# Performance work log

Measured on AMD Instinct MI355X. Metric: run time of the kernel, lower is better.

Reference implementation:

```python
import jax, jax.numpy as jnp
import numpy as np

S_LIST = (0.015, 0.02, 0.04, 0.08)
EPS = 1e-6
LOG_EPS = float(np.log(EPS))


def _ema_filtfilt(x, s):
    """scipy.signal.filtfilt([s], [1, s-1], x, axis=-1, padtype=None).

    Forward pass: y[n] = (1-s)*y[n-1] + s*x[n], with scipy's lfilter_zi*x[0]
    initial condition, which makes y[0] = x[0] exactly. Then the same filter
    is run backward (flip, filter, flip), again with y2[0] = (flipped y)[0].
    Implemented as a parallel linear-recurrence via associative_scan.
    """
    def one_pass(v):
        a = jnp.full_like(v, 1.0 - s).at[..., 0].set(0.0)
        b = (s * v).at[..., 0].set(v[..., 0])
        def comb(c1, c2):
            a1, b1 = c1
            a2, b2 = c2
            return a1 * a2, b1 * a2 + b2
        _, y = jax.lax.associative_scan(comb, (a, b), axis=-1)
        return y

    y = one_pass(x)                       # forward
    y = jnp.flip(one_pass(jnp.flip(y, axis=-1)), axis=-1)  # backward
    return y


def setup_inputs() -> dict:
    key = jax.random.key(0)
    ks = jax.random.split(key, 5)
    B, C, F, T = 16, 1, 256, 4096
    K = len(S_LIST)
    x = jax.random.uniform(ks[0], (B, C, F, T), dtype=jnp.float32)
    log_alpha = jnp.log(jax.random.normal(ks[1], (F,), dtype=jnp.float32) * 0.1 + 1.0)
    log_delta = jnp.log(jax.random.normal(ks[2], (F,), dtype=jnp.float32) * 0.1 + 1.0)
    log_r = jnp.log(jax.random.normal(ks[3], (F,), dtype=jnp.float32) * 0.1 + 1.0)
    z_ks = jax.random.normal(ks[4], (K, F), dtype=jnp.float32) * 0.1 + np.log(1.0 / K)
    return {"x": x, "log_alpha": log_alpha, "log_delta": log_delta,
            "log_r": log_r, "z_ks": z_ks}


def reference(x, log_alpha, log_delta, log_r, z_ks):
    # per-frequency params broadcast over [B, C, F, T]
    alpha = jnp.exp(log_alpha)[None, None, :, None]
    delta = jnp.exp(log_delta)[None, None, :, None]
    r = jnp.exp(log_r)[None, None, :, None]
    ez = jnp.exp(z_ks)
    w_ks = ez / jnp.sum(ez)  # [K, F], normalized over ALL entries (as in source)

    # multi-scale filtfilt smoothers; scipy path is detached from autodiff
    smoothers = jnp.stack([_ema_filtfilt(x, s) for s in S_LIST])  # [K,B,C,F,T]
    smoothers = jax.lax.stop_gradient(smoothers)

    M = jnp.einsum('kf,kbcft->bcft', w_ks, smoothers)
    M = jnp.exp(-alpha * (LOG_EPS + jnp.log1p(M / EPS)))
    return (x * M + delta) ** r - delta ** r
```

## Files before the change

kernel.cpp:

```cpp
#include <hip/hip_runtime.h>
#include <math.h>

#define T_DIM 4096
#define F_DIM 256
#define NROWS 4096
#define CHUNK 16
#define LOG2E 1.4426950408889634f

typedef float v2f __attribute__((ext_vector_type(2)));

__device__ __forceinline__ float fexp2(float v) { return __builtin_amdgcn_exp2f(v); }
__device__ __forceinline__ float flog2(float v) { return __builtin_amdgcn_logf(v); }
__device__ __forceinline__ float fexp(float v)  { return fexp2(v * LOG2E); }

__host__ __device__ constexpr float cpow(float b, int e) {
    float r = 1.0f;
    for (int i = 0; i < e; ++i) r *= b;
    return r;
}

template<int N> struct PT { float v[N]; };
template<int N>
__host__ __device__ constexpr PT<N> mk_pows(float a) {
    PT<N> t{}; float p = 1.0f;
    for (int i = 0; i < N; ++i) { t.v[i] = p; p *= a; }
    return t;
}

__device__ __forceinline__ v2f shfl_up2(v2f v, int d) {
    v2f r; r.x = __shfl_up(v.x, d, 64); r.y = __shfl_up(v.y, d, 64); return r;
}
__device__ __forceinline__ v2f shfl_down2(v2f v, int d) {
    v2f r; r.x = __shfl_down(v.x, d, 64); r.y = __shfl_down(v.y, d, 64); return r;
}

template<int K0, int K1>
__device__ __forceinline__ void smooth_pair(const float xv[CHUNK], v2f y[CHUNK],
                                            int tid, int lane, int wid, v2f* sE)
{
    constexpr float SL0 = (K0==0)?0.015f:(K0==1)?0.02f:(K0==2)?0.04f:0.08f;
    constexpr float SL1 = (K1==0)?0.015f:(K1==1)?0.02f:(K1==2)?0.04f:0.08f;
    constexpr float a0 = 1.0f - SL0, a1 = 1.0f - SL1;
    constexpr float A0 = cpow(a0, CHUNK), A1 = cpow(a1, CHUNK);
    constexpr float A64_0 = cpow(a0, 64*CHUNK), A64_1 = cpow(a1, 64*CHUNK);
    constexpr PT<CHUNK+1> P0 = mk_pows<CHUNK+1>(a0);
    constexpr PT<CHUNK+1> P1 = mk_pows<CHUNK+1>(a1);
    constexpr PT<33> PA0 = mk_pows<33>(A0);
    constexpr PT<33> PA1 = mk_pows<33>(A1);

    const v2f av = {a0, a1};
    const v2f sv = {SL0, SL1};
    const v2f A64v = {A64_0, A64_1};
    const float lgA0 = flog2(A0), lgA1 = flog2(A1);
    const v2f zero = {0.0f, 0.0f};

    {
        v2f x0 = {xv[0], xv[0]};
        y[0] = (tid == 0) ? x0 : (sv * x0);
    }
    #pragma unroll
    for (int i = 1; i < CHUNK; ++i) {
        v2f xi = {xv[i], xv[i]};
        y[i] = av * y[i-1] + sv * xi;
    }
    {
        v2f e = y[CHUNK-1];
        #pragma unroll
        for (int st = 0; st < 6; ++st) {
            const int d = 1 << st;
            const v2f Ad = {PA0.v[d], PA1.v[d]};
            v2f t = shfl_up2(e, d);
            if (lane >= d) e = Ad * t + e;
        }
        __syncthreads();
        if (lane == 63) sE[wid] = e;
        __syncthreads();
        v2f C = zero;
        for (int j = 0; j < wid; ++j) C = A64v * C + sE[j];
        v2f eex = shfl_up2(e, 1);
        v2f cprev = (lane == 0) ? zero : eex;
        const float fl = (float)lane;
        v2f pAl = {fexp2(fl * lgA0), fexp2(fl * lgA1)};
        v2f c = cprev + pAl * C;
        #pragma unroll
        for (int i = 0; i < CHUNK; ++i) {
            const v2f ap = {P0.v[i+1], P1.v[i+1]};
            y[i] = ap * c + y[i];
        }
    }

    y[CHUNK-1] = (tid == 255) ? y[CHUNK-1] : (sv * y[CHUNK-1]);
    #pragma unroll
    for (int i = CHUNK-2; i >= 0; --i) y[i] = av * y[i+1] + sv * y[i];
    {
        v2f e = y[0];
        #pragma unroll
        for (int st = 0; st < 6; ++st) {
            const int d = 1 << st;
            const v2f Ad = {PA0.v[d], PA1.v[d]};
            v2f t = shfl_down2(e, d);
            if (lane < 64 - d) e = Ad * t + e;
        }
        __syncthreads();
        if (lane == 0) sE[wid] = e;
        __syncthreads();
        v2f C = zero;
        for (int j = 3; j > wid; --j) C = A64v * C + sE[j];
        v2f eex = shfl_down2(e, 1);
        v2f cnext = (lane == 63) ? zero : eex;
        const float frl = (float)(63 - lane);
        v2f pAr = {fexp2(frl * lgA0), fexp2(frl * lgA1)};
        v2f c = cnext + pAr * C;
        #pragma unroll
        for (int i = CHUNK-1; i >= 0; --i) {
            const v2f ap = {P0.v[CHUNK-i], P1.v[CHUNK-i]};
            y[i] = ap * c + y[i];
        }
    }
}

__global__ __launch_bounds__(256, 4)
void pcen_kernel(const float* __restrict__ x,
                 const float* __restrict__ log_alpha,
                 const float* __restrict__ log_delta,
                 const float* __restrict__ log_r,
                 const float* __restrict__ z_ks,
                 float* __restrict__ out)
{
    const int tid  = threadIdx.x;
    const int lane = tid & 63;
    const int wid  = tid >> 6;
    const int rid  = blockIdx.x;
    const int f    = rid & (F_DIM - 1);

    __shared__ float sred[4];
    __shared__ v2f   sE[4];
    __shared__ float sSum;

    float zs = fexp(z_ks[tid])       + fexp(z_ks[tid + 256])
             + fexp(z_ks[tid + 512]) + fexp(z_ks[tid + 768]);
    #pragma unroll
    for (int d = 32; d >= 1; d >>= 1) zs += __shfl_down(zs, d, 64);
    if (lane == 0) sred[wid] = zs;
    __syncthreads();
    if (tid == 0) sSum = sred[0] + sred[1] + sred[2] + sred[3];
    __syncthreads();
    const float invsum = 1.0f / sSum;

    float wk[4];
    #pragma unroll
    for (int k = 0; k < 4; ++k) wk[k] = fexp(z_ks[k * F_DIM + f]) * invsum;
    const float alpha = fexp(log_alpha[f]);
    const float delta = fexp(log_delta[f]);
    const float rr    = fexp(log_r[f]);
    const float dr    = fexp2(rr * flog2(delta));
    const float nalpha = -alpha;

    const size_t base = (size_t)rid * T_DIM + (size_t)tid * CHUNK;
    float xv[CHUNK];
    {
        const float4* xp = (const float4*)(x + base);
        #pragma unroll
        for (int j = 0; j < 4; ++j) {
            float4 v = xp[j];
            xv[4*j+0] = v.x; xv[4*j+1] = v.y; xv[4*j+2] = v.z; xv[4*j+3] = v.w;
        }
    }

    v2f y[CHUNK];
    v2f Mpk[CHUNK];

    smooth_pair<0,1>(xv, y, tid, lane, wid, sE);
    {
        const v2f wv = {wk[0], wk[1]};
        #pragma unroll
        for (int i = 0; i < CHUNK; ++i) Mpk[i] = wv * y[i];
    }
    smooth_pair<2,3>(xv, y, tid, lane, wid, sE);
    {
        const v2f wv = {wk[2], wk[3]};
        #pragma unroll
        for (int i = 0; i < CHUNK; ++i) Mpk[i] = wv * y[i] + Mpk[i];
    }

    float4* op = (float4*)(out + base);
    #pragma unroll
    for (int j = 0; j < 4; ++j) {
        float o[4];
        #pragma unroll
        for (int q = 0; q < 4; ++q) {
            const int i = 4*j + q;
            const float M  = Mpk[i].x + Mpk[i].y;
            const float Mp = fexp2(nalpha * flog2(M + 1.0e-6f));
            const float v  = fmaf(xv[i], Mp, delta);
            o[q] = fexp2(rr * flog2(v)) - dr;
        }
        op[j] = make_float4(o[0], o[1], o[2], o[3]);
    }
}

extern "C" void kernel_launch(void* const* d_in, const int* in_sizes, int n_in,
                              void* d_out, int out_size, void* d_ws, size_t ws_size,
                              hipStream_t stream) {
    const float* x  = (const float*)d_in[0];
    const float* la = (const float*)d_in[1];
    const float* ld = (const float*)d_in[2];
    const float* lr = (const float*)d_in[3];
    const float* zk = (const float*)d_in[4];
    float* o = (float*)d_out;
    (void)in_sizes; (void)n_in; (void)out_size; (void)d_ws; (void)ws_size;
    hipLaunchKernelGGL(pcen_kernel, dim3(NROWS), dim3(256), 0, stream,
                       x, la, ld, lr, zk, o);
}
```

Measured before the change: 39.27 us.

## Interleave all four EMA smoother scans in one pass and hoist input loads

Runs the two smoother pairs side by side instead of one after the other, so the forward and backward scans, shuffles and cross-wave combines happen once for all four scales. This halves the block barriers and doubles independent work per instruction to hide shuffle latency. It also issues the global x loads before the z_ks softmax reduction to overlap memory latency, and drops the first barrier before the forward-pass shared write. The cost is more live registers (two y arrays) at 4 waves per SIMD occupancy.

```diff
diff --git a/kernel.cpp b/kernel.cpp
--- a/kernel.cpp
+++ b/kernel.cpp
@@ -34,90 +34,10 @@
     v2f r; r.x = __shfl_down(v.x, d, 64); r.y = __shfl_down(v.y, d, 64); return r;
 }
 
-template<int K0, int K1>
-__device__ __forceinline__ void smooth_pair(const float xv[CHUNK], v2f y[CHUNK],
-                                            int tid, int lane, int wid, v2f* sE)
-{
-    constexpr float SL0 = (K0==0)?0.015f:(K0==1)?0.02f:(K0==2)?0.04f:0.08f;
-    constexpr float SL1 = (K1==0)?0.015f:(K1==1)?0.02f:(K1==2)?0.04f:0.08f;
-    constexpr float a0 = 1.0f - SL0, a1 = 1.0f - SL1;
-    constexpr float A0 = cpow(a0, CHUNK), A1 = cpow(a1, CHUNK);
-    constexpr float A64_0 = cpow(a0, 64*CHUNK), A64_1 = cpow(a1, 64*CHUNK);
-    constexpr PT<CHUNK+1> P0 = mk_pows<CHUNK+1>(a0);
-    constexpr PT<CHUNK+1> P1 = mk_pows<CHUNK+1>(a1);
-    constexpr PT<33> PA0 = mk_pows<33>(A0);
-    constexpr PT<33> PA1 = mk_pows<33>(A1);
-
-    const v2f av = {a0, a1};
-    const v2f sv = {SL0, SL1};
-    const v2f A64v = {A64_0, A64_1};
-    const float lgA0 = flog2(A0), lgA1 = flog2(A1);
-    const v2f zero = {0.0f, 0.0f};
-
-    {
-        v2f x0 = {xv[0], xv[0]};
-        y[0] = (tid == 0) ? x0 : (sv * x0);
-    }
-    #pragma unroll
-    for (int i = 1; i < CHUNK; ++i) {
-        v2f xi = {xv[i], xv[i]};
-        y[i] = av * y[i-1] + sv * xi;
-    }
-    {
-        v2f e = y[CHUNK-1];
-        #pragma unroll
-        for (int st = 0; st < 6; ++st) {
-            const int d = 1 << st;
-            const v2f Ad = {PA0.v[d], PA1.v[d]};
-            v2f t = shfl_up2(e, d);
-            if (lane >= d) e = Ad * t + e;
-        }
-        __syncthreads();
-        if (lane == 63) sE[wid] = e;
-        __syncthreads();
-        v2f C = zero;
-        for (int j = 0; j < wid; ++j) C = A64v * C + sE[j];
-        v2f eex = shfl_up2(e, 1);
-        v2f cprev = (lane == 0) ? zero : eex;
-        const float fl = (float)lane;
-        v2f pAl = {fexp2(fl * lgA0), fexp2(fl * lgA1)};
-        v2f c = cprev + pAl * C;
-        #pragma unroll
-        for (int i = 0; i < CHUNK; ++i) {
-            const v2f ap = {P0.v[i+1], P1.v[i+1]};
-            y[i] = ap * c + y[i];
-        }
-    }
-
-    y[CHUNK-1] = (tid == 255) ? y[CHUNK-1] : (sv * y[CHUNK-1]);
-    #pragma unroll
-    for (int i = CHUNK-2; i >= 0; --i) y[i] = av * y[i+1] + sv * y[i];
-    {
-        v2f e = y[0];
-        #pragma unroll
-        for (int st = 0; st < 6; ++st) {
-            const int d = 1 << st;
-            const v2f Ad = {PA0.v[d], PA1.v[d]};
-            v2f t = shfl_down2(e, d);
-            if (lane < 64 - d) e = Ad * t + e;
-        }
-        __syncthreads();
-        if (lane == 0) sE[wid] = e;
-        __syncthreads();
-        v2f C = zero;
-        for (int j = 3; j > wid; --j) C = A64v * C + sE[j];
-        v2f eex = shfl_down2(e, 1);
-        v2f cnext = (lane == 63) ? zero : eex;
-        const float frl = (float)(63 - lane);
-        v2f pAr = {fexp2(frl * lgA0), fexp2(frl * lgA1)};
-        v2f c = cnext + pAr * C;
-        #pragma unroll
-        for (int i = CHUNK-1; i >= 0; --i) {
-            const v2f ap = {P0.v[CHUNK-i], P1.v[CHUNK-i]};
-            y[i] = ap * c + y[i];
-        }
-    }
-}
+#define S0 0.015f
+#define S1 0.02f
+#define S2 0.04f
+#define S3 0.08f
 
 __global__ __launch_bounds__(256, 4)
 void pcen_kernel(const float* __restrict__ x,
@@ -134,8 +54,13 @@
     const int f    = rid & (F_DIM - 1);
 
     __shared__ float sred[4];
-    __shared__ v2f   sE[4];
+    __shared__ v2f   sE0[4];
+    __shared__ v2f   sE1[4];
     __shared__ float sSum;
+
+    const size_t base = (size_t)rid * T_DIM + (size_t)tid * CHUNK;
+    const float4* xp = (const float4*)(x + base);
+    float4 xq0 = xp[0], xq1 = xp[1], xq2 = xp[2], xq3 = xp[3];
 
     float zs = fexp(z_ks[tid])       + fexp(z_ks[tid + 256])
              + fexp(z_ks[tid + 512]) + fexp(z_ks[tid + 768]);
@@ -156,41 +81,133 @@
     const float dr    = fexp2(rr * flog2(delta));
     const float nalpha = -alpha;
 
-    const size_t base = (size_t)rid * T_DIM + (size_t)tid * CHUNK;
     float xv[CHUNK];
+    xv[0]=xq0.x; xv[1]=xq0.y; xv[2]=xq0.z; xv[3]=xq0.w;
+    xv[4]=xq1.x; xv[5]=xq1.y; xv[6]=xq1.z; xv[7]=xq1.w;
+    xv[8]=xq2.x; xv[9]=xq2.y; xv[10]=xq2.z; xv[11]=xq2.w;
+    xv[12]=xq3.x; xv[13]=xq3.y; xv[14]=xq3.z; xv[15]=xq3.w;
+
+    constexpr float a0 = 1.0f - S0, a1 = 1.0f - S1, a2 = 1.0f - S2, a3 = 1.0f - S3;
+    constexpr float A0 = cpow(a0, CHUNK), A1 = cpow(a1, CHUNK);
+    constexpr float A2 = cpow(a2, CHUNK), A3 = cpow(a3, CHUNK);
+    constexpr float A64_0 = cpow(a0, 64*CHUNK), A64_1 = cpow(a1, 64*CHUNK);
+    constexpr float A64_2 = cpow(a2, 64*CHUNK), A64_3 = cpow(a3, 64*CHUNK);
+    constexpr PT<CHUNK+1> P0 = mk_pows<CHUNK+1>(a0);
+    constexpr PT<CHUNK+1> P1 = mk_pows<CHUNK+1>(a1);
+    constexpr PT<CHUNK+1> P2 = mk_pows<CHUNK+1>(a2);
+    constexpr PT<CHUNK+1> P3 = mk_pows<CHUNK+1>(a3);
+    constexpr PT<33> PA0 = mk_pows<33>(A0);
+    constexpr PT<33> PA1 = mk_pows<33>(A1);
+    constexpr PT<33> PA2 = mk_pows<33>(A2);
+    constexpr PT<33> PA3 = mk_pows<33>(A3);
+
+    const v2f av01 = {a0, a1}, av23 = {a2, a3};
+    const v2f sv01 = {S0, S1}, sv23 = {S2, S3};
+    const v2f A64v01 = {A64_0, A64_1}, A64v23 = {A64_2, A64_3};
+    const float lgA0 = flog2(A0), lgA1 = flog2(A1), lgA2 = flog2(A2), lgA3 = flog2(A3);
+    const v2f zero = {0.0f, 0.0f};
+
+    v2f y0[CHUNK], y1[CHUNK];
+
     {
-        const float4* xp = (const float4*)(x + base);
-        #pragma unroll
-        for (int j = 0; j < 4; ++j) {
-            float4 v = xp[j];
-            xv[4*j+0] = v.x; xv[4*j+1] = v.y; xv[4*j+2] = v.z; xv[4*j+3] = v.w;
-        }
-    }
-
-    v2f y[CHUNK];
-    v2f Mpk[CHUNK];
-
-    smooth_pair<0,1>(xv, y, tid, lane, wid, sE);
+        v2f x0v = {xv[0], xv[0]};
+        y0[0] = (tid == 0) ? x0v : (sv01 * x0v);
+        y1[0] = (tid == 0) ? x0v : (sv23 * x0v);
+    }
+    #pragma unroll
+    for (int i = 1; i < CHUNK; ++i) {
+        v2f xi = {xv[i], xv[i]};
+        y0[i] = av01 * y0[i-1] + sv01 * xi;
+        y1[i] = av23 * y1[i-1] + sv23 * xi;
+    }
     {
-        const v2f wv = {wk[0], wk[1]};
-        #pragma unroll
-        for (int i = 0; i < CHUNK; ++i) Mpk[i] = wv * y[i];
-    }
-    smooth_pair<2,3>(xv, y, tid, lane, wid, sE);
+        v2f e0 = y0[CHUNK-1], e1 = y1[CHUNK-1];
+        #pragma unroll
+        for (int st = 0; st < 6; ++st) {
+            const int d = 1 << st;
+            const v2f Ad01 = {PA0.v[d], PA1.v[d]};
+            const v2f Ad23 = {PA2.v[d], PA3.v[d]};
+            v2f t0 = shfl_up2(e0, d);
+            v2f t1 = shfl_up2(e1, d);
+            if (lane >= d) { e0 = Ad01 * t0 + e0; e1 = Ad23 * t1 + e1; }
+        }
+        if (lane == 63) { sE0[wid] = e0; sE1[wid] = e1; }
+        __syncthreads();
+        v2f C0 = zero, C1 = zero;
+        for (int j = 0; j < wid; ++j) {
+            C0 = A64v01 * C0 + sE0[j];
+            C1 = A64v23 * C1 + sE1[j];
+        }
+        v2f ex0 = shfl_up2(e0, 1), ex1 = shfl_up2(e1, 1);
+        v2f cp0 = (lane == 0) ? zero : ex0;
+        v2f cp1 = (lane == 0) ? zero : ex1;
+        const float fl = (float)lane;
+        v2f pAl01 = {fexp2(fl * lgA0), fexp2(fl * lgA1)};
+        v2f pAl23 = {fexp2(fl * lgA2), fexp2(fl * lgA3)};
+        v2f c0 = cp0 + pAl01 * C0;
+        v2f c1 = cp1 + pAl23 * C1;
+        #pragma unroll
+        for (int i = 0; i < CHUNK; ++i) {
+            const v2f ap01 = {P0.v[i+1], P1.v[i+1]};
+            const v2f ap23 = {P2.v[i+1], P3.v[i+1]};
+            y0[i] = ap01 * c0 + y0[i];
+            y1[i] = ap23 * c1 + y1[i];
+        }
+    }
+
+    y0[CHUNK-1] = (tid == 255) ? y0[CHUNK-1] : (sv01 * y0[CHUNK-1]);
+    y1[CHUNK-1] = (tid == 255) ? y1[CHUNK-1] : (sv23 * y1[CHUNK-1]);
+    #pragma unroll
+    for (int i = CHUNK-2; i >= 0; --i) {
+        y0[i] = av01 * y0[i+1] + sv01 * y0[i];
+        y1[i] = av23 * y1[i+1] + sv23 * y1[i];
+    }
     {
-        const v2f wv = {wk[2], wk[3]};
-        #pragma unroll
-        for (int i = 0; i < CHUNK; ++i) Mpk[i] = wv * y[i] + Mpk[i];
+        v2f e0 = y0[0], e1 = y1[0];
+        #pragma unroll
+        for (int st = 0; st < 6; ++st) {
+            const int d = 1 << st;
+            const v2f Ad01 = {PA0.v[d], PA1.v[d]};
+            const v2f Ad23 = {PA2.v[d], PA3.v[d]};
+            v2f t0 = shfl_down2(e0, d);
+            v2f t1 = shfl_down2(e1, d);
+            if (lane < 64 - d) { e0 = Ad01 * t0 + e0; e1 = Ad23 * t1 + e1; }
+        }
+        __syncthreads();
+        if (lane == 0) { sE0[wid] = e0; sE1[wid] = e1; }
+        __syncthreads();
+        v2f C0 = zero, C1 = zero;
+        for (int j = 3; j > wid; --j) {
+            C0 = A64v01 * C0 + sE0[j];
+            C1 = A64v23 * C1 + sE1[j];
+        }
+        v2f ex0 = shfl_down2(e0, 1), ex1 = shfl_down2(e1, 1);
+        v2f cn0 = (lane == 63) ? zero : ex0;
+        v2f cn1 = (lane == 63) ? zero : ex1;
+        const float frl = (float)(63 - lane);
+        v2f pAr01 = {fexp2(frl * lgA0), fexp2(frl * lgA1)};
+        v2f pAr23 = {fexp2(frl * lgA2), fexp2(frl * lgA3)};
+        v2f c0 = cn0 + pAr01 * C0;
+        v2f c1 = cn1 + pAr23 * C1;
+        #pragma unroll
+        for (int i = CHUNK-1; i >= 0; --i) {
+            const v2f ap01 = {P0.v[CHUNK-i], P1.v[CHUNK-i]};
+            const v2f ap23 = {P2.v[CHUNK-i], P3.v[CHUNK-i]};
+            y0[i] = ap01 * c0 + y0[i];
+            y1[i] = ap23 * c1 + y1[i];
+        }
     }
 
     float4* op = (float4*)(out + base);
+    const v2f wv01 = {wk[0], wk[1]}, wv23 = {wk[2], wk[3]};
     #pragma unroll
     for (int j = 0; j < 4; ++j) {
         float o[4];
         #pragma unroll
         for (int q = 0; q < 4; ++q) {
             const int i = 4*j + q;
-            const float M  = Mpk[i].x + Mpk[i].y;
+            v2f mp = wv01 * y0[i] + wv23 * y1[i];
+            const float M  = mp.x + mp.y;
             const float Mp = fexp2(nalpha * flog2(M + 1.0e-6f));
             const float v  = fmaf(xv[i], Mp, delta);
             o[q] = fexp2(rr * flog2(v)) - dr;
```

Measured after the change: 35.68 us. 1.1x faster.
